# Kernel tuning notes

Measured on AMD Instinct MI355X. Metric: run time of the kernel, lower is better.

The kernel has to match this reference:

```python
import jax, jax.numpy as jnp
import numpy as np

N = 100000      # num nodes
E = 1000000     # num edges
D_IN = 64
D_OUT = 64


def setup_inputs() -> dict:
    key = jax.random.key(0)
    k1, k2, k3, k4 = jax.random.split(key, 4)
    x = jax.random.normal(k1, (N, D_IN), dtype=jnp.float32)
    edge_index = jax.random.randint(k2, (2, E), 0, N, dtype=jnp.int32)
    weight = jax.random.normal(k3, (D_OUT, D_IN), dtype=jnp.float32) / np.float32(np.sqrt(D_IN))
    bias = jax.random.normal(k4, (D_OUT,), dtype=jnp.float32) * 0.01
    return {"x": x, "edge_index": edge_index, "weight": weight, "bias": bias}


def reference(x, edge_index, weight, bias):
    # GCNConv forward: remove self loops (as weight-0 edges for static shapes),
    # add self loops, symmetric degree normalization, linear, gather-scatter aggregate.
    n = x.shape[0]
    src, dst = edge_index[0], edge_index[1]
    keep = (src != dst).astype(x.dtype)          # filtered self-loops get weight 0
    loop = jnp.arange(n, dtype=src.dtype)
    row = jnp.concatenate([src, loop])           # [E+N] source (gather) index
    col = jnp.concatenate([dst, loop])           # [E+N] destination (scatter) index
    ew = jnp.concatenate([keep, jnp.ones((n,), x.dtype)])

    deg = jax.ops.segment_sum(ew, col, num_segments=n)            # [N]
    dis = jnp.where(deg > 0, jax.lax.rsqrt(deg), 0.0)             # deg^-0.5, inf->0
    norm = dis[row] * ew * dis[col]                               # [E+N]

    h = x @ weight.T                                              # [N, D_OUT]
    msgs = norm[:, None] * h[row]                                 # [E+N, D_OUT]
    out = jax.ops.segment_sum(msgs, col, num_segments=n)          # [N, D_OUT]
    return out + bias
```

## Files before the change

### kernel.cpp

```cpp
#include <hip/hip_runtime.h>
#include <hip/hip_bf16.h>

static constexpr int N = 100000;
static constexpr int E = 1000000;
static constexpr int D = 64;
static constexpr int NB = 391;
static constexpr int CAP = 3072;
static constexpr int PART_EPT = 8;
static constexpr int PART_CHUNK = 256 * PART_EPT;
static constexpr int PART_BLOCKS = (E + PART_CHUNK - 1) / PART_CHUNK;

typedef __attribute__((ext_vector_type(8))) short bf16x8;
typedef __attribute__((ext_vector_type(4))) float f32x4;

__device__ inline ushort f2bf(float f) {
    unsigned u = __float_as_uint(f);
    return (ushort)((u + 0x7fffu + ((u >> 16) & 1u)) >> 16);
}

__global__ __launch_bounds__(256) void k_part(const int* __restrict__ ei,
                                              const float* __restrict__ w,
                                              int* __restrict__ gcur,
                                              int* __restrict__ part,
                                              ushort* __restrict__ wbf) {
    __shared__ int hcnt[NB];
    __shared__ int hcur[NB];
    int tid = threadIdx.x;
    if (blockIdx.x == 0) {
        int i0 = tid * 16;
#pragma unroll
        for (int c = 0; c < 4; ++c) {
            float4 v = *reinterpret_cast<const float4*>(w + i0 + c * 4);
            ushort4 o;
            o.x = f2bf(v.x); o.y = f2bf(v.y); o.z = f2bf(v.z); o.w = f2bf(v.w);
            *reinterpret_cast<ushort4*>(wbf + i0 + c * 4) = o;
        }
    }
    for (int b = tid; b < NB; b += 256) hcnt[b] = 0;
    __syncthreads();
    int base = blockIdx.x * PART_CHUNK + tid;
    int ss[PART_EPT], tt[PART_EPT];
#pragma unroll
    for (int k = 0; k < PART_EPT; ++k) {
        int i = base + k * 256;
        int s = -1, t = 0;
        if (i < E) {
            s = ei[i];
            t = ei[E + i];
            if (s == t) s = -1;
        }
        ss[k] = s; tt[k] = t;
        if (s >= 0) atomicAdd(&hcnt[t >> 8], 1);
    }
    __syncthreads();
    for (int b = tid; b < NB; b += 256) {
        int c = hcnt[b];
        hcur[b] = b * CAP + (c ? atomicAdd(&gcur[b], c) : 0);
    }
    __syncthreads();
#pragma unroll
    for (int k = 0; k < PART_EPT; ++k) {
        int s = ss[k];
        if (s >= 0) {
            int b = tt[k] >> 8;
            int pos = atomicAdd(&hcur[b], 1);
            if (pos < (b + 1) * CAP)
                part[pos] = s | ((tt[k] & 255) << 17);
        }
    }
}

__global__ __launch_bounds__(512) void k_csr(const int* __restrict__ gcur,
                                             const int* __restrict__ part,
                                             int* __restrict__ cnt,
                                             int* __restrict__ row_start,
                                             int* __restrict__ srcs) {
    __shared__ int cntL[256];
    __shared__ int scanL[256];
    __shared__ int curL[256];
    int tid = threadIdx.x;
    int b = blockIdx.x;
    if (tid < 256) cntL[tid] = 0;
    __syncthreads();
    int en = gcur[b];
    en = en < CAP ? en : CAP;
    const int* pb = part + b * CAP;
    for (int i = tid; i < en; i += 512)
        atomicAdd(&cntL[pb[i] >> 17], 1);
    __syncthreads();
    if (tid < 256) scanL[tid] = cntL[tid];
    __syncthreads();
    for (int off = 1; off < 256; off <<= 1) {
        int v = 0;
        if (tid < 256 && tid >= off) v = scanL[tid - off];
        __syncthreads();
        if (tid < 256) scanL[tid] += v;
        __syncthreads();
    }
    if (tid < 256) {
        int node = b * 256 + tid;
        int excl = scanL[tid] - cntL[tid];
        if (node < N) {
            row_start[node] = b * CAP + excl;
            cnt[node] = cntL[tid];
        }
        curL[tid] = excl;
    }
    __syncthreads();
    for (int i = tid; i < en; i += 512) {
        int e = pb[i];
        int pos = atomicAdd(&curL[e >> 17], 1);
        srcs[b * CAP + pos] = e & 0x1FFFF;
    }
}

__global__ __launch_bounds__(256) void k_linear(const float* __restrict__ x,
                                                const ushort* __restrict__ wbf,
                                                const int* __restrict__ cnt,
                                                ushort* __restrict__ hb) {
    int tid = threadIdx.x;
    if (blockIdx.x == 0 && tid < 32)
        reinterpret_cast<int*>(hb + N * D)[tid] = 0;
    int lane = tid & 63, wave = tid >> 6;
    int tbase = blockIdx.x * 64 + wave * 16;
    if (tbase >= N) return;
    int r15 = lane & 15, g4 = lane >> 4;
    int arow = tbase + r15;
    if (arow >= N) arow = N - 1;
    bf16x8 afr[2];
#pragma unroll
    for (int ks = 0; ks < 2; ++ks) {
        const float* ap = x + arow * 64 + ks * 32 + g4 * 8;
        float4 v0 = *reinterpret_cast<const float4*>(ap);
        float4 v1 = *reinterpret_cast<const float4*>(ap + 4);
        bf16x8 a;
        a[0] = (short)f2bf(v0.x); a[1] = (short)f2bf(v0.y);
        a[2] = (short)f2bf(v0.z); a[3] = (short)f2bf(v0.w);
        a[4] = (short)f2bf(v1.x); a[5] = (short)f2bf(v1.y);
        a[6] = (short)f2bf(v1.z); a[7] = (short)f2bf(v1.w);
        afr[ks] = a;
    }
    f32x4 acc[4] = {};
#pragma unroll
    for (int nt = 0; nt < 4; ++nt)
#pragma unroll
        for (int ks = 0; ks < 2; ++ks) {
            bf16x8 b = *reinterpret_cast<const bf16x8*>(
                wbf + (nt * 16 + r15) * 64 + ks * 32 + g4 * 8);
            acc[nt] = __builtin_amdgcn_mfma_f32_16x16x32_bf16(afr[ks], b, acc[nt], 0, 0, 0);
        }
#pragma unroll
    for (int r = 0; r < 4; ++r) {
        int node = tbase + g4 * 4 + r;
        if (node < N) {
            float dt = rsqrtf((float)(cnt[node] + 1));
#pragma unroll
            for (int nt = 0; nt < 4; ++nt)
                hb[node * D + nt * 16 + r15] = f2bf(dt * acc[nt][r]);
        }
    }
}

#define ACC8(v)                                                    \
    acc[0] += __uint_as_float(((unsigned)(v).x) << 16);            \
    acc[1] += __uint_as_float(((unsigned)(v).x) & 0xffff0000u);    \
    acc[2] += __uint_as_float(((unsigned)(v).y) << 16);            \
    acc[3] += __uint_as_float(((unsigned)(v).y) & 0xffff0000u);    \
    acc[4] += __uint_as_float(((unsigned)(v).z) << 16);            \
    acc[5] += __uint_as_float(((unsigned)(v).z) & 0xffff0000u);    \
    acc[6] += __uint_as_float(((unsigned)(v).w) << 16);            \
    acc[7] += __uint_as_float(((unsigned)(v).w) & 0xffff0000u);

__global__ __launch_bounds__(256) void k_agg(const int* __restrict__ row_start,
                                             const int* __restrict__ cnt,
                                             const int* __restrict__ srcs,
                                             const ushort* __restrict__ hb,
                                             const float* __restrict__ bias,
                                             float* __restrict__ out) {
    int g = blockIdx.x * 256 + threadIdx.x;
    int t = g >> 6, lane = g & 63;
    if (t >= N) return;
    int q = lane >> 3, l = lane & 7;
    int base = row_start[t];
    int len = cnt[t];
    float acc[8];
#pragma unroll
    for (int i = 0; i < 8; ++i) acc[i] = 0.f;

    int s0 = (q < len) ? srcs[base + q] : N;
    int4 v = *reinterpret_cast<const int4*>(hb + s0 * D + l * 8);
    for (int k0 = 8; k0 < len; k0 += 8) {
        int idx = k0 + q;
        int s1 = (idx < len) ? srcs[base + idx] : N;
        int4 vn = *reinterpret_cast<const int4*>(hb + s1 * D + l * 8);
        ACC8(v);
        v = vn;
    }
    ACC8(v);

#pragma unroll
    for (int i = 0; i < 8; ++i) {
        acc[i] += __shfl_down(acc[i], 32);
        acc[i] += __shfl_down(acc[i], 16);
        acc[i] += __shfl_down(acc[i], 8);
    }
    if (lane < 8) {
        int4 vt = *reinterpret_cast<const int4*>(hb + t * D + lane * 8);
        ACC8(vt);
        float dt = rsqrtf((float)(len + 1));
        float4 ba = *reinterpret_cast<const float4*>(&bias[lane * 8]);
        float4 bb = *reinterpret_cast<const float4*>(&bias[lane * 8 + 4]);
        float4 o0, o1;
        o0.x = fmaf(dt, acc[0], ba.x);
        o0.y = fmaf(dt, acc[1], ba.y);
        o0.z = fmaf(dt, acc[2], ba.z);
        o0.w = fmaf(dt, acc[3], ba.w);
        o1.x = fmaf(dt, acc[4], bb.x);
        o1.y = fmaf(dt, acc[5], bb.y);
        o1.z = fmaf(dt, acc[6], bb.z);
        o1.w = fmaf(dt, acc[7], bb.w);
        *reinterpret_cast<float4*>(out + t * D + lane * 8) = o0;
        *reinterpret_cast<float4*>(out + t * D + lane * 8 + 4) = o1;
    }
}

extern "C" void kernel_launch(void* const* d_in, const int* in_sizes, int n_in,
                              void* d_out, int out_size, void* d_ws, size_t ws_size,
                              hipStream_t stream) {
    const float* x    = (const float*)d_in[0];
    const int*   ei   = (const int*)d_in[1];
    const float* w    = (const float*)d_in[2];
    const float* bias = (const float*)d_in[3];
    float* out = (float*)d_out;

    char* ws = (char*)d_ws;
    int*    gcur = (int*)(ws);
    ushort* wbf  = (ushort*)(ws + 1664);
    int*    part = (int*)(ws + 9856);
    int*    srcs = (int*)(ws + 4814464);
    int*    cnt  = (int*)(ws + 9619072);
    int*    rs   = (int*)(ws + 10019072);
    ushort* hb   = (ushort*)(ws + 10419072);

    hipMemsetAsync(gcur, 0, 1664, stream);
    k_part  <<<PART_BLOCKS, 256, 0, stream>>>(ei, w, gcur, part, wbf);
    k_csr   <<<NB, 512, 0, stream>>>(gcur, part, cnt, rs, srcs);
    k_linear<<<(N + 63) / 64, 256, 0, stream>>>(x, wbf, cnt, hb);
    k_agg   <<<(N * 64) / 256, 256, 0, stream>>>(rs, cnt, srcs, hb, bias, out);
}
```

Measured before the change: 88.77 us.

## Fuse partition and linear kernels, apply source degree scaling in aggregation

The dst-degree scaling of h is moved out of the linear transform: h is stored unscaled, a per-node dis array is computed in the CSR kernel, and the aggregation multiplies each gathered row by dis[src] with FMAs. This removes the dependency of the linear transform on the degree counts, so the linear transform now runs inside the edge-partition kernel as extra blocks. The memset is replaced by a tiny init kernel that also converts the weights. In exchange, aggregation does an extra scattered 4-byte load per edge, and the bf16 rounding now happens before scaling rather than after.

New measurement: 83.39 us. -6.1%, faster.

```diff
diff --git a/kernel.cpp b/kernel.cpp
--- a/kernel.cpp
+++ b/kernel.cpp
@@ -9,6 +9,7 @@
 static constexpr int PART_EPT = 8;
 static constexpr int PART_CHUNK = 256 * PART_EPT;
 static constexpr int PART_BLOCKS = (E + PART_CHUNK - 1) / PART_CHUNK;
+static constexpr int LIN_BLOCKS = (N + 63) / 64;
 
 typedef __attribute__((ext_vector_type(8))) short bf16x8;
 typedef __attribute__((ext_vector_type(4))) float f32x4;
@@ -18,54 +19,104 @@
     return (ushort)((u + 0x7fffu + ((u >> 16) & 1u)) >> 16);
 }
 
-__global__ __launch_bounds__(256) void k_part(const int* __restrict__ ei,
-                                              const float* __restrict__ w,
+__global__ __launch_bounds__(256) void k_init(const float* __restrict__ w,
                                               int* __restrict__ gcur,
-                                              int* __restrict__ part,
-                                              ushort* __restrict__ wbf) {
+                                              float* __restrict__ dis,
+                                              ushort* __restrict__ wbf,
+                                              ushort* __restrict__ hb) {
+    int tid = threadIdx.x;
+    int i0 = tid * 16;
+#pragma unroll
+    for (int c = 0; c < 4; ++c) {
+        float4 v = *reinterpret_cast<const float4*>(w + i0 + c * 4);
+        ushort4 o;
+        o.x = f2bf(v.x); o.y = f2bf(v.y); o.z = f2bf(v.z); o.w = f2bf(v.w);
+        *reinterpret_cast<ushort4*>(wbf + i0 + c * 4) = o;
+    }
+    for (int b = tid; b < NB; b += 256) gcur[b] = 0;
+    if (tid == 0) dis[N] = 0.f;
+    if (tid < 32) reinterpret_cast<int*>(hb + N * D)[tid] = 0;
+}
+
+__global__ __launch_bounds__(256) void k_partlin(const int* __restrict__ ei,
+                                                 const float* __restrict__ x,
+                                                 const ushort* __restrict__ wbf,
+                                                 int* __restrict__ gcur,
+                                                 int* __restrict__ part,
+                                                 ushort* __restrict__ hb) {
     __shared__ int hcnt[NB];
     __shared__ int hcur[NB];
     int tid = threadIdx.x;
-    if (blockIdx.x == 0) {
-        int i0 = tid * 16;
-#pragma unroll
-        for (int c = 0; c < 4; ++c) {
-            float4 v = *reinterpret_cast<const float4*>(w + i0 + c * 4);
-            ushort4 o;
-            o.x = f2bf(v.x); o.y = f2bf(v.y); o.z = f2bf(v.z); o.w = f2bf(v.w);
-            *reinterpret_cast<ushort4*>(wbf + i0 + c * 4) = o;
-        }
-    }
-    for (int b = tid; b < NB; b += 256) hcnt[b] = 0;
-    __syncthreads();
-    int base = blockIdx.x * PART_CHUNK + tid;
-    int ss[PART_EPT], tt[PART_EPT];
-#pragma unroll
-    for (int k = 0; k < PART_EPT; ++k) {
-        int i = base + k * 256;
-        int s = -1, t = 0;
-        if (i < E) {
-            s = ei[i];
-            t = ei[E + i];
-            if (s == t) s = -1;
-        }
-        ss[k] = s; tt[k] = t;
-        if (s >= 0) atomicAdd(&hcnt[t >> 8], 1);
-    }
-    __syncthreads();
-    for (int b = tid; b < NB; b += 256) {
-        int c = hcnt[b];
-        hcur[b] = b * CAP + (c ? atomicAdd(&gcur[b], c) : 0);
-    }
-    __syncthreads();
-#pragma unroll
-    for (int k = 0; k < PART_EPT; ++k) {
-        int s = ss[k];
-        if (s >= 0) {
-            int b = tt[k] >> 8;
-            int pos = atomicAdd(&hcur[b], 1);
-            if (pos < (b + 1) * CAP)
-                part[pos] = s | ((tt[k] & 255) << 17);
+    if (blockIdx.x < PART_BLOCKS) {
+        for (int b = tid; b < NB; b += 256) hcnt[b] = 0;
+        __syncthreads();
+        int base = blockIdx.x * PART_CHUNK + tid;
+        int ss[PART_EPT], tt[PART_EPT];
+#pragma unroll
+        for (int k = 0; k < PART_EPT; ++k) {
+            int i = base + k * 256;
+            int s = -1, t = 0;
+            if (i < E) {
+                s = ei[i];
+                t = ei[E + i];
+                if (s == t) s = -1;
+            }
+            ss[k] = s; tt[k] = t;
+            if (s >= 0) atomicAdd(&hcnt[t >> 8], 1);
+        }
+        __syncthreads();
+        for (int b = tid; b < NB; b += 256) {
+            int c = hcnt[b];
+            hcur[b] = b * CAP + (c ? atomicAdd(&gcur[b], c) : 0);
+        }
+        __syncthreads();
+#pragma unroll
+        for (int k = 0; k < PART_EPT; ++k) {
+            int s = ss[k];
+            if (s >= 0) {
+                int b = tt[k] >> 8;
+                int pos = atomicAdd(&hcur[b], 1);
+                if (pos < (b + 1) * CAP)
+                    part[pos] = s | ((tt[k] & 255) << 17);
+            }
+        }
+    } else {
+        int lane = tid & 63, wave = tid >> 6;
+        int tbase = (blockIdx.x - PART_BLOCKS) * 64 + wave * 16;
+        if (tbase >= N) return;
+        int r15 = lane & 15, g4 = lane >> 4;
+        int arow = tbase + r15;
+        if (arow >= N) arow = N - 1;
+        bf16x8 afr[2];
+#pragma unroll
+        for (int ks = 0; ks < 2; ++ks) {
+            const float* ap = x + arow * 64 + ks * 32 + g4 * 8;
+            float4 v0 = *reinterpret_cast<const float4*>(ap);
+            float4 v1 = *reinterpret_cast<const float4*>(ap + 4);
+            bf16x8 a;
+            a[0] = (short)f2bf(v0.x); a[1] = (short)f2bf(v0.y);
+            a[2] = (short)f2bf(v0.z); a[3] = (short)f2bf(v0.w);
+            a[4] = (short)f2bf(v1.x); a[5] = (short)f2bf(v1.y);
+            a[6] = (short)f2bf(v1.z); a[7] = (short)f2bf(v1.w);
+            afr[ks] = a;
+        }
+        f32x4 acc[4] = {};
+#pragma unroll
+        for (int nt = 0; nt < 4; ++nt)
+#pragma unroll
+            for (int ks = 0; ks < 2; ++ks) {
+                bf16x8 b = *reinterpret_cast<const bf16x8*>(
+                    wbf + (nt * 16 + r15) * 64 + ks * 32 + g4 * 8);
+                acc[nt] = __builtin_amdgcn_mfma_f32_16x16x32_bf16(afr[ks], b, acc[nt], 0, 0, 0);
+            }
+#pragma unroll
+        for (int r = 0; r < 4; ++r) {
+            int node = tbase + g4 * 4 + r;
+            if (node < N) {
+#pragma unroll
+                for (int nt = 0; nt < 4; ++nt)
+                    hb[node * D + nt * 16 + r15] = f2bf(acc[nt][r]);
+            }
         }
     }
 }
@@ -74,7 +125,8 @@
                                              const int* __restrict__ part,
                                              int* __restrict__ cnt,
                                              int* __restrict__ row_start,
-                                             int* __restrict__ srcs) {
+                                             int* __restrict__ srcs,
+                                             float* __restrict__ dis) {
     __shared__ int cntL[256];
     __shared__ int scanL[256];
     __shared__ int curL[256];
@@ -103,6 +155,7 @@
         if (node < N) {
             row_start[node] = b * CAP + excl;
             cnt[node] = cntL[tid];
+            dis[node] = rsqrtf((float)(cntL[tid] + 1));
         }
         curL[tid] = excl;
     }
@@ -114,67 +167,21 @@
     }
 }
 
-__global__ __launch_bounds__(256) void k_linear(const float* __restrict__ x,
-                                                const ushort* __restrict__ wbf,
-                                                const int* __restrict__ cnt,
-                                                ushort* __restrict__ hb) {
-    int tid = threadIdx.x;
-    if (blockIdx.x == 0 && tid < 32)
-        reinterpret_cast<int*>(hb + N * D)[tid] = 0;
-    int lane = tid & 63, wave = tid >> 6;
-    int tbase = blockIdx.x * 64 + wave * 16;
-    if (tbase >= N) return;
-    int r15 = lane & 15, g4 = lane >> 4;
-    int arow = tbase + r15;
-    if (arow >= N) arow = N - 1;
-    bf16x8 afr[2];
-#pragma unroll
-    for (int ks = 0; ks < 2; ++ks) {
-        const float* ap = x + arow * 64 + ks * 32 + g4 * 8;
-        float4 v0 = *reinterpret_cast<const float4*>(ap);
-        float4 v1 = *reinterpret_cast<const float4*>(ap + 4);
-        bf16x8 a;
-        a[0] = (short)f2bf(v0.x); a[1] = (short)f2bf(v0.y);
-        a[2] = (short)f2bf(v0.z); a[3] = (short)f2bf(v0.w);
-        a[4] = (short)f2bf(v1.x); a[5] = (short)f2bf(v1.y);
-        a[6] = (short)f2bf(v1.z); a[7] = (short)f2bf(v1.w);
-        afr[ks] = a;
-    }
-    f32x4 acc[4] = {};
-#pragma unroll
-    for (int nt = 0; nt < 4; ++nt)
-#pragma unroll
-        for (int ks = 0; ks < 2; ++ks) {
-            bf16x8 b = *reinterpret_cast<const bf16x8*>(
-                wbf + (nt * 16 + r15) * 64 + ks * 32 + g4 * 8);
-            acc[nt] = __builtin_amdgcn_mfma_f32_16x16x32_bf16(afr[ks], b, acc[nt], 0, 0, 0);
-        }
-#pragma unroll
-    for (int r = 0; r < 4; ++r) {
-        int node = tbase + g4 * 4 + r;
-        if (node < N) {
-            float dt = rsqrtf((float)(cnt[node] + 1));
-#pragma unroll
-            for (int nt = 0; nt < 4; ++nt)
-                hb[node * D + nt * 16 + r15] = f2bf(dt * acc[nt][r]);
-        }
-    }
-}
-
-#define ACC8(v)                                                    \
-    acc[0] += __uint_as_float(((unsigned)(v).x) << 16);            \
-    acc[1] += __uint_as_float(((unsigned)(v).x) & 0xffff0000u);    \
-    acc[2] += __uint_as_float(((unsigned)(v).y) << 16);            \
-    acc[3] += __uint_as_float(((unsigned)(v).y) & 0xffff0000u);    \
-    acc[4] += __uint_as_float(((unsigned)(v).z) << 16);            \
-    acc[5] += __uint_as_float(((unsigned)(v).z) & 0xffff0000u);    \
-    acc[6] += __uint_as_float(((unsigned)(v).w) << 16);            \
-    acc[7] += __uint_as_float(((unsigned)(v).w) & 0xffff0000u);
+#define FMACC8(d, v)                                                        \
+    acc[0] = fmaf(d, __uint_as_float(((unsigned)(v).x) << 16), acc[0]);     \
+    acc[1] = fmaf(d, __uint_as_float(((unsigned)(v).x) & 0xffff0000u), acc[1]); \
+    acc[2] = fmaf(d, __uint_as_float(((unsigned)(v).y) << 16), acc[2]);     \
+    acc[3] = fmaf(d, __uint_as_float(((unsigned)(v).y) & 0xffff0000u), acc[3]); \
+    acc[4] = fmaf(d, __uint_as_float(((unsigned)(v).z) << 16), acc[4]);     \
+    acc[5] = fmaf(d, __uint_as_float(((unsigned)(v).z) & 0xffff0000u), acc[5]); \
+    acc[6] = fmaf(d, __uint_as_float(((unsigned)(v).w) << 16), acc[6]);     \
+    acc[7] = fmaf(d, __uint_as_float(((unsigned)(v).w) & 0xffff0000u), acc[7]);
 
 __global__ __launch_bounds__(256) void k_agg(const int* __restrict__ row_start,
                                              const int* __restrict__ cnt,
                                              const int* __restrict__ srcs,
                                              const ushort* __restrict__ hb,
+                                             const float* __restrict__ dis,
                                              const float* __restrict__ bias,
                                              float* __restrict__ out) {
     int g = blockIdx.x * 256 + threadIdx.x;
@@ -188,15 +195,17 @@
     for (int i = 0; i < 8; ++i) acc[i] = 0.f;
 
     int s0 = (q < len) ? srcs[base + q] : N;
+    float d0 = dis[s0];
     int4 v = *reinterpret_cast<const int4*>(hb + s0 * D + l * 8);
     for (int k0 = 8; k0 < len; k0 += 8) {
         int idx = k0 + q;
         int s1 = (idx < len) ? srcs[base + idx] : N;
+        float d1 = dis[s1];
         int4 vn = *reinterpret_cast<const int4*>(hb + s1 * D + l * 8);
-        ACC8(v);
-        v = vn;
-    }
-    ACC8(v);
+        FMACC8(d0, v);
+        d0 = d1; v = vn;
+    }
+    FMACC8(d0, v);
 
 #pragma unroll
     for (int i = 0; i < 8; ++i) {
@@ -205,9 +214,9 @@
         acc[i] += __shfl_down(acc[i], 8);
     }
     if (lane < 8) {
+        float dt = rsqrtf((float)(len + 1));
         int4 vt = *reinterpret_cast<const int4*>(hb + t * D + lane * 8);
-        ACC8(vt);
-        float dt = rsqrtf((float)(len + 1));
+        FMACC8(dt, vt);
         float4 ba = *reinterpret_cast<const float4*>(&bias[lane * 8]);
         float4 bb = *reinterpret_cast<const float4*>(&bias[lane * 8 + 4]);
         float4 o0, o1;
@@ -240,11 +249,11 @@
     int*    srcs = (int*)(ws + 4814464);
     int*    cnt  = (int*)(ws + 9619072);
     int*    rs   = (int*)(ws + 10019072);
-    ushort* hb   = (ushort*)(ws + 10419072);
-
-    hipMemsetAsync(gcur, 0, 1664, stream);
-    k_part  <<<PART_BLOCKS, 256, 0, stream>>>(ei, w, gcur, part, wbf);
-    k_csr   <<<NB, 512, 0, stream>>>(gcur, part, cnt, rs, srcs);
-    k_linear<<<(N + 63) / 64, 256, 0, stream>>>(x, wbf, cnt, hb);
-    k_agg   <<<(N * 64) / 256, 256, 0, stream>>>(rs, cnt, srcs, hb, bias, out);
-}
+    float*  dis  = (float*)(ws + 10419072);
+    ushort* hb   = (ushort*)(ws + 10819200);
+
+    k_init   <<<1, 256, 0, stream>>>(w, gcur, dis, wbf, hb);
+    k_partlin<<<PART_BLOCKS + LIN_BLOCKS, 256, 0, stream>>>(ei, x, wbf, gcur, part, hb);
+    k_csr    <<<NB, 512, 0, stream>>>(gcur, part, cnt, rs, srcs, dis);
+    k_agg    <<<(N * 64) / 256, 256, 0, stream>>>(rs, cnt, srcs, hb, dis, bias, out);
+}
```
